# Kernel tuning notes

Measured on AMD Instinct MI355X. Metric: run time of the kernel, lower is better.

Reference implementation:

```python
import jax, jax.numpy as jnp
import numpy as np

T, H, F, E, K = 2048, 1024, 1024, 8, 2  # tokens, hidden, ffn, experts, top_k


def setup_inputs() -> dict:
    key = jax.random.key(0)
    k1, k2, k3, k4, k5 = jax.random.split(key, 5)
    hidden_states = jax.random.normal(k1, (T, H), dtype=jnp.float32)
    # router outputs: positive weights (renormalize=False in module, used as-is)
    topk_weights = jax.random.uniform(k2, (T, K), dtype=jnp.float32)
    topk_ids = jax.random.randint(k3, (T, K), 0, E, dtype=jnp.int32)
    # gate_up: (E, 2F, H) with first F rows = gate, last F rows = up
    gate_up_weight = jax.random.normal(k4, (E, 2 * F, H), dtype=jnp.float32) * 0.02
    # down: (E, H, F)
    down_weight = jax.random.normal(k5, (E, H, F), dtype=jnp.float32) * 0.02
    return {
        'hidden_states': hidden_states,
        'topk_weights': topk_weights,
        'topk_ids': topk_ids,
        'gate_up_weight': gate_up_weight,
        'down_weight': down_weight,
    }


def reference(hidden_states, topk_weights, topk_ids, gate_up_weight, down_weight):
    # Fused MoE: per selected expert, y = (silu(x@Wg^T) * (x@Wu^T)) @ Wd^T,
    # combined with router weights (renormalize=False).
    f = down_weight.shape[-1]
    # [T, E, 2F]: gate_up projection for every expert (dense ref for grouped GEMM)
    gu = jnp.einsum('th,eoh->teo', hidden_states, gate_up_weight)
    gate, up = gu[..., :f], gu[..., f:]
    act = jax.nn.silu(gate) * up                     # [T, E, F]
    y = jnp.einsum('tef,ehf->teh', act, down_weight)  # [T, E, H]
    # gather the top-k experts per token and combine
    y_sel = jnp.take_along_axis(y, topk_ids[:, :, None], axis=1)  # [T, K, H]
    out = jnp.sum(y_sel * topk_weights[:, :, None], axis=1)       # [T, H]
    return out.astype(hidden_states.dtype)
```

## Files before the change

### kernel.cpp

```cpp
#include <hip/hip_runtime.h>
#include <hip/hip_bf16.h>

#define T_TOK 2048
#define HID   1024
#define FF    1024
#define NEXP  8
#define NPAIR 4096

#define BM 128
#define BN 64
#define BK 32
#define MAX_MT 40
#define MAXROWS (MAX_MT*BM)
#define PPT (NPAIR/256)

using bf16x8 = __attribute__((ext_vector_type(8))) __bf16;
using f32x4  = __attribute__((ext_vector_type(4))) float;

__device__ __forceinline__ unsigned short f2bf(float f) {
    unsigned int u = __float_as_uint(f);
    return (unsigned short)((u + 0x7FFF + ((u >> 16) & 1)) >> 16);
}
__device__ __forceinline__ float bf2f(unsigned short s) {
    return __uint_as_float(((unsigned int)s) << 16);
}
__device__ __forceinline__ void gll16(const unsigned short* g, unsigned short* l) {
    __builtin_amdgcn_global_load_lds(
        (const __attribute__((address_space(1))) void*)(const void*)g,
        (__attribute__((address_space(3))) void*)(void*)l, 16, 0, 0);
}

__global__ void prep_kernel(const float* __restrict__ wgu,
                            const float* __restrict__ wdn,
                            const float* __restrict__ hs,
                            const int* __restrict__ ids,
                            int* __restrict__ pair_pos,
                            int* __restrict__ row_tok,
                            int* __restrict__ meta,
                            unsigned short* __restrict__ wgu_b,
                            unsigned short* __restrict__ wdn_b,
                            unsigned short* __restrict__ hs_b) {
    int tid = threadIdx.x;
    if (blockIdx.x == 2048) {
        __shared__ int S[2][256][NEXP];
        __shared__ int base[NEXP];
        int myc[NEXP];
        int eloc[PPT];
#pragma unroll
        for (int e = 0; e < NEXP; e++) myc[e] = 0;
#pragma unroll
        for (int i = 0; i < PPT; i++) {
            int e = ids[tid * PPT + i];
            eloc[i] = e;
#pragma unroll
            for (int ee = 0; ee < NEXP; ee++) myc[ee] += (e == ee);
        }
#pragma unroll
        for (int e = 0; e < NEXP; e++) S[0][tid][e] = myc[e];
        __syncthreads();
        int src = 0;
        for (int d = 1; d < 256; d <<= 1) {
#pragma unroll
            for (int e = 0; e < NEXP; e++) {
                int v = S[src][tid][e];
                if (tid >= d) v += S[src][tid - d][e];
                S[src ^ 1][tid][e] = v;
            }
            __syncthreads();
            src ^= 1;
        }
        if (tid == 0) {
            int mt = 0;
            for (int e = 0; e < NEXP; e++) {
                meta[e] = mt;
                base[e] = mt * BM;
                mt += (S[src][255][e] + BM - 1) / BM;
            }
            meta[NEXP] = mt;
        }
        for (int i = tid; i < MAXROWS; i += 256) row_tok[i] = -1;
        __syncthreads();
        int off[NEXP];
#pragma unroll
        for (int e = 0; e < NEXP; e++) off[e] = base[e] + S[src][tid][e] - myc[e];
#pragma unroll
        for (int i = 0; i < PPT; i++) {
            int p = tid * PPT + i;
            int e = eloc[i];
            int pos = 0;
#pragma unroll
            for (int ee = 0; ee < NEXP; ee++) if (e == ee) pos = off[ee]++;
            pair_pos[p] = pos;
            row_tok[pos] = p >> 1;
        }
        return;
    }
    long stride = 2048L * 256;
    long t0 = (long)blockIdx.x * 256 + tid;
    const long NW1 = (long)NEXP * 2 * FF * HID / 4;
    for (long i = t0; i < NW1; i += stride) {
        float4 v = ((const float4*)wgu)[i];
        ushort4 o; o.x = f2bf(v.x); o.y = f2bf(v.y); o.z = f2bf(v.z); o.w = f2bf(v.w);
        ((ushort4*)wgu_b)[i] = o;
    }
    const long NW2 = (long)NEXP * HID * FF / 4;
    for (long i = t0; i < NW2; i += stride) {
        float4 v = ((const float4*)wdn)[i];
        ushort4 o; o.x = f2bf(v.x); o.y = f2bf(v.y); o.z = f2bf(v.z); o.w = f2bf(v.w);
        ((ushort4*)wdn_b)[i] = o;
    }
    const long NH = (long)T_TOK * HID / 4;
    for (long i = t0; i < NH; i += stride) {
        float4 v = ((const float4*)hs)[i];
        ushort4 o; o.x = f2bf(v.x); o.y = f2bf(v.y); o.z = f2bf(v.z); o.w = f2bf(v.w);
        ((ushort4*)hs_b)[i] = o;
    }
}

template<int EPI, int NBY>
__global__ __launch_bounds__(256)
void gemm_moe(const unsigned short* __restrict__ A,
              const unsigned short* __restrict__ B,
              unsigned short* __restrict__ Cbf,
              const int* __restrict__ meta,
              const int* __restrict__ row_tok,
              int K, long Bexp) {
    __shared__ unsigned short As[2][BM * BK];
    __shared__ unsigned short Bs[2][BN * BK];

    int L = blockIdx.x;
    int xcd = L & 7;
    int slot = L >> 3;
    constexpr int PER = NBY / 8;
    int by = xcd * PER + (slot % PER);
    int bx = slot / PER;
    if (bx >= meta[NEXP]) return;
    int e = 0;
#pragma unroll
    for (int i = 1; i < NEXP; i++) if (bx >= meta[i]) e = i;

    long m0 = (long)bx * BM;
    int n0 = by * BN;
    const unsigned short* Bb = B + (long)e * Bexp;

    int tid = threadIdx.x, lane = tid & 63, wv = tid >> 6;
    const int r = lane & 15;
    const int q = lane >> 4;
    const int mw = (wv >> 1) * 64, nw = (wv & 1) * 32;
    const int sw = (q ^ ((r >> 1) & 3)) * 8;

    const unsigned short* ap[2];
#pragma unroll
    for (int h = 0; h < 2; h++) {
        int c = h * 256 + tid;
        int row = c >> 2, cp = c & 3;
        int cc = cp ^ ((row >> 1) & 3);
        long grow;
        if (EPI == 1) {
            int tk = row_tok[m0 + row];
            if (tk < 0) tk = 0;
            grow = tk;
        } else {
            grow = m0 + row;
        }
        ap[h] = A + grow * (long)K + cc * 8;
    }
    const unsigned short* bp;
    {
        int c = tid;
        int row = c >> 2, cp = c & 3;
        int cc = cp ^ ((row >> 1) & 3);
        long grow;
        if (EPI == 1) grow = ((row & 1) ? FF : 0) + ((n0 + row) >> 1);
        else          grow = n0 + row;
        bp = Bb + grow * (long)K + cc * 8;
    }

    auto stage = [&](int s, int k0) {
#pragma unroll
        for (int h = 0; h < 2; h++)
            gll16(ap[h] + k0, &As[s][(h * 256 + tid) * 8]);
        gll16(bp + k0, &Bs[s][tid * 8]);
    };

    f32x4 acc[4][2] = {};
    const int NKI = K / BK;
    stage(0, 0);
    for (int ki = 0; ki < NKI; ki++) {
        __syncthreads();
        if (ki + 1 < NKI) stage((ki + 1) & 1, (ki + 1) * BK);
        int s = ki & 1;
        bf16x8 a[4], b[2];
#pragma unroll
        for (int i = 0; i < 4; i++)
            a[i] = *(const bf16x8*)&As[s][(mw + i * 16 + r) * BK + sw];
#pragma unroll
        for (int j = 0; j < 2; j++)
            b[j] = *(const bf16x8*)&Bs[s][(nw + j * 16 + r) * BK + sw];
#pragma unroll
        for (int i = 0; i < 4; i++)
#pragma unroll
            for (int j = 0; j < 2; j++)
                acc[i][j] = __builtin_amdgcn_mfma_f32_16x16x32_bf16(a[i], b[j], acc[i][j], 0, 0, 0);
        __syncthreads();
    }

    if (EPI == 1) {
#pragma unroll
        for (int i = 0; i < 4; i++) {
            long rowb = m0 + mw + i * 16 + q * 4;
#pragma unroll
            for (int j = 0; j < 2; j++) {
                int n = n0 + nw + j * 16 + r;
#pragma unroll
                for (int reg = 0; reg < 4; reg++) {
                    float v = acc[i][j][reg];
                    float o = __shfl_xor(v, 1);
                    if (!(r & 1)) {
                        float g = v, u = o;
                        float s2 = g / (1.f + __expf(-g)) * u;
                        Cbf[(rowb + reg) * (long)FF + (n >> 1)] = f2bf(s2);
                    }
                }
            }
        }
    } else {
#pragma unroll
        for (int i = 0; i < 4; i++) {
            long rowb = m0 + mw + i * 16 + q * 4;
#pragma unroll
            for (int j = 0; j < 2; j++) {
                int n = n0 + nw + j * 16 + r;
#pragma unroll
                for (int reg = 0; reg < 4; reg++)
                    Cbf[(rowb + reg) * (long)HID + n] = f2bf(acc[i][j][reg]);
            }
        }
    }
}

__global__ void combine_kernel(const unsigned short* __restrict__ y,
                               const float* __restrict__ tw,
                               const int* __restrict__ pair_pos,
                               float* __restrict__ out) {
    int t = blockIdx.x;
    int c = threadIdx.x * 4;
    int p0 = pair_pos[t * 2], p1 = pair_pos[t * 2 + 1];
    float w0 = tw[t * 2], w1 = tw[t * 2 + 1];
    ushort4 a = *(const ushort4*)(y + (long)p0 * HID + c);
    ushort4 b = *(const ushort4*)(y + (long)p1 * HID + c);
    float4 o;
    o.x = w0 * bf2f(a.x) + w1 * bf2f(b.x);
    o.y = w0 * bf2f(a.y) + w1 * bf2f(b.y);
    o.z = w0 * bf2f(a.z) + w1 * bf2f(b.z);
    o.w = w0 * bf2f(a.w) + w1 * bf2f(b.w);
    *(float4*)(out + (long)t * HID + c) = o;
}

extern "C" void kernel_launch(void* const* d_in, const int* in_sizes, int n_in,
                              void* d_out, int out_size, void* d_ws, size_t ws_size,
                              hipStream_t stream) {
    const float* hs  = (const float*)d_in[0];
    const float* tw  = (const float*)d_in[1];
    const int*   ids = (const int*)d_in[2];
    const float* wgu = (const float*)d_in[3];
    const float* wdn = (const float*)d_in[4];
    float* out = (float*)d_out;

    char* ws = (char*)d_ws;
    size_t off = 0;
    auto alloc = [&](size_t bytes) -> void* {
        void* p = ws + off;
        off += (bytes + 255) & ~(size_t)255;
        return p;
    };
    unsigned short* wgu_b = (unsigned short*)alloc((size_t)NEXP * 2 * FF * HID * 2);
    unsigned short* wdn_b = (unsigned short*)alloc((size_t)NEXP * HID * FF * 2);
    unsigned short* hs_b  = (unsigned short*)alloc((size_t)T_TOK * HID * 2);
    unsigned short* act   = (unsigned short*)alloc((size_t)MAXROWS * FF * 2);
    unsigned short* ybuf  = (unsigned short*)alloc((size_t)MAXROWS * HID * 2);
    int* pair_pos = (int*)alloc(NPAIR * 4);
    int* row_tok  = (int*)alloc(MAXROWS * 4);
    int* meta     = (int*)alloc(64);

    prep_kernel<<<2049, 256, 0, stream>>>(wgu, wdn, hs, ids,
                                          pair_pos, row_tok, meta,
                                          wgu_b, wdn_b, hs_b);

    gemm_moe<1, 32><<<32 * MAX_MT, 256, 0, stream>>>(
        hs_b, wgu_b, act, meta, row_tok, HID, (long)(2 * FF) * HID);

    gemm_moe<2, 16><<<16 * MAX_MT, 256, 0, stream>>>(
        act, wdn_b, ybuf, meta, row_tok, FF, (long)HID * FF);

    combine_kernel<<<T_TOK, 256, 0, stream>>>(ybuf, tw, pair_pos, out);
}
```

Baseline: 205.6 us.

## Fuse fp32 weight-to-bf16 conversion into GEMM loads and widen N tile

```diff
diff --git a/kernel.cpp b/kernel.cpp
--- a/kernel.cpp
+++ b/kernel.cpp
@@ -8,13 +8,15 @@
 #define NPAIR 4096
 
 #define BM 128
-#define BN 64
+#define BN 128
 #define BK 32
 #define MAX_MT 40
 #define MAXROWS (MAX_MT*BM)
 #define PPT (NPAIR/256)
+#define NPREP 512
 
 using bf16x8 = __attribute__((ext_vector_type(8))) __bf16;
+using us8    = __attribute__((ext_vector_type(8))) unsigned short;
 using f32x4  = __attribute__((ext_vector_type(4))) float;
 
 __device__ __forceinline__ unsigned short f2bf(float f) {
@@ -24,24 +26,15 @@
 __device__ __forceinline__ float bf2f(unsigned short s) {
     return __uint_as_float(((unsigned int)s) << 16);
 }
-__device__ __forceinline__ void gll16(const unsigned short* g, unsigned short* l) {
-    __builtin_amdgcn_global_load_lds(
-        (const __attribute__((address_space(1))) void*)(const void*)g,
-        (__attribute__((address_space(3))) void*)(void*)l, 16, 0, 0);
-}
-
-__global__ void prep_kernel(const float* __restrict__ wgu,
-                            const float* __restrict__ wdn,
-                            const float* __restrict__ hs,
+
+__global__ void prep_kernel(const float* __restrict__ hs,
                             const int* __restrict__ ids,
                             int* __restrict__ pair_pos,
                             int* __restrict__ row_tok,
                             int* __restrict__ meta,
-                            unsigned short* __restrict__ wgu_b,
-                            unsigned short* __restrict__ wdn_b,
                             unsigned short* __restrict__ hs_b) {
     int tid = threadIdx.x;
-    if (blockIdx.x == 2048) {
+    if (blockIdx.x == NPREP) {
         __shared__ int S[2][256][NEXP];
         __shared__ int base[NEXP];
         int myc[NEXP];
@@ -95,22 +88,9 @@
         }
         return;
     }
-    long stride = 2048L * 256;
-    long t0 = (long)blockIdx.x * 256 + tid;
-    const long NW1 = (long)NEXP * 2 * FF * HID / 4;
-    for (long i = t0; i < NW1; i += stride) {
-        float4 v = ((const float4*)wgu)[i];
-        ushort4 o; o.x = f2bf(v.x); o.y = f2bf(v.y); o.z = f2bf(v.z); o.w = f2bf(v.w);
-        ((ushort4*)wgu_b)[i] = o;
-    }
-    const long NW2 = (long)NEXP * HID * FF / 4;
-    for (long i = t0; i < NW2; i += stride) {
-        float4 v = ((const float4*)wdn)[i];
-        ushort4 o; o.x = f2bf(v.x); o.y = f2bf(v.y); o.z = f2bf(v.z); o.w = f2bf(v.w);
-        ((ushort4*)wdn_b)[i] = o;
-    }
+    long stride = (long)NPREP * 256;
     const long NH = (long)T_TOK * HID / 4;
-    for (long i = t0; i < NH; i += stride) {
+    for (long i = (long)blockIdx.x * 256 + tid; i < NH; i += stride) {
         float4 v = ((const float4*)hs)[i];
         ushort4 o; o.x = f2bf(v.x); o.y = f2bf(v.y); o.z = f2bf(v.z); o.w = f2bf(v.w);
         ((ushort4*)hs_b)[i] = o;
@@ -120,7 +100,7 @@
 template<int EPI, int NBY>
 __global__ __launch_bounds__(256)
 void gemm_moe(const unsigned short* __restrict__ A,
-              const unsigned short* __restrict__ B,
+              const float* __restrict__ Bf,
               unsigned short* __restrict__ Cbf,
               const int* __restrict__ meta,
               const int* __restrict__ row_tok,
@@ -141,68 +121,79 @@
 
     long m0 = (long)bx * BM;
     int n0 = by * BN;
-    const unsigned short* Bb = B + (long)e * Bexp;
 
     int tid = threadIdx.x, lane = tid & 63, wv = tid >> 6;
     const int r = lane & 15;
     const int q = lane >> 4;
-    const int mw = (wv >> 1) * 64, nw = (wv & 1) * 32;
+    const int mw = (wv >> 1) * 64, nw = (wv & 1) * 64;
     const int sw = (q ^ ((r >> 1) & 3)) * 8;
 
-    const unsigned short* ap[2];
+    const unsigned short* apb[2];
+    const float* bpb[2];
 #pragma unroll
     for (int h = 0; h < 2; h++) {
         int c = h * 256 + tid;
         int row = c >> 2, cp = c & 3;
         int cc = cp ^ ((row >> 1) & 3);
-        long grow;
+        long ga, gb;
         if (EPI == 1) {
             int tk = row_tok[m0 + row];
             if (tk < 0) tk = 0;
-            grow = tk;
+            ga = tk;
+            gb = ((row & 1) ? FF : 0) + ((n0 + row) >> 1);
         } else {
-            grow = m0 + row;
-        }
-        ap[h] = A + grow * (long)K + cc * 8;
-    }
-    const unsigned short* bp;
-    {
-        int c = tid;
-        int row = c >> 2, cp = c & 3;
-        int cc = cp ^ ((row >> 1) & 3);
-        long grow;
-        if (EPI == 1) grow = ((row & 1) ? FF : 0) + ((n0 + row) >> 1);
-        else          grow = n0 + row;
-        bp = Bb + grow * (long)K + cc * 8;
-    }
-
-    auto stage = [&](int s, int k0) {
-#pragma unroll
-        for (int h = 0; h < 2; h++)
-            gll16(ap[h] + k0, &As[s][(h * 256 + tid) * 8]);
-        gll16(bp + k0, &Bs[s][tid * 8]);
+            ga = m0 + row;
+            gb = n0 + row;
+        }
+        apb[h] = A + ga * (long)K + cc * 8;
+        bpb[h] = Bf + (long)e * Bexp + gb * (long)K + cc * 8;
+    }
+
+    us8   Ar[2];
+    float4 Br[2][2];
+    auto ldregs = [&](int k0) {
+#pragma unroll
+        for (int h = 0; h < 2; h++) {
+            Ar[h]    = *(const us8*)(apb[h] + k0);
+            Br[h][0] = *(const float4*)(bpb[h] + k0);
+            Br[h][1] = *(const float4*)(bpb[h] + k0 + 4);
+        }
     };
-
-    f32x4 acc[4][2] = {};
+    auto dswrite = [&](int s) {
+#pragma unroll
+        for (int h = 0; h < 2; h++) {
+            int c = h * 256 + tid;
+            *(us8*)&As[s][c * 8] = Ar[h];
+            us8 bo;
+            float4 x = Br[h][0], y = Br[h][1];
+            bo[0] = f2bf(x.x); bo[1] = f2bf(x.y); bo[2] = f2bf(x.z); bo[3] = f2bf(x.w);
+            bo[4] = f2bf(y.x); bo[5] = f2bf(y.y); bo[6] = f2bf(y.z); bo[7] = f2bf(y.w);
+            *(us8*)&Bs[s][c * 8] = bo;
+        }
+    };
+
+    f32x4 acc[4][4] = {};
     const int NKI = K / BK;
-    stage(0, 0);
+    ldregs(0);
+    dswrite(0);
+    ldregs(BK);
     for (int ki = 0; ki < NKI; ki++) {
         __syncthreads();
-        if (ki + 1 < NKI) stage((ki + 1) & 1, (ki + 1) * BK);
         int s = ki & 1;
-        bf16x8 a[4], b[2];
+        bf16x8 a[4], b[4];
 #pragma unroll
         for (int i = 0; i < 4; i++)
             a[i] = *(const bf16x8*)&As[s][(mw + i * 16 + r) * BK + sw];
 #pragma unroll
-        for (int j = 0; j < 2; j++)
+        for (int j = 0; j < 4; j++)
             b[j] = *(const bf16x8*)&Bs[s][(nw + j * 16 + r) * BK + sw];
+        if (ki + 1 < NKI) dswrite(s ^ 1);
+        if (ki + 2 < NKI) ldregs((ki + 2) * BK);
 #pragma unroll
         for (int i = 0; i < 4; i++)
 #pragma unroll
-            for (int j = 0; j < 2; j++)
+            for (int j = 0; j < 4; j++)
                 acc[i][j] = __builtin_amdgcn_mfma_f32_16x16x32_bf16(a[i], b[j], acc[i][j], 0, 0, 0);
-        __syncthreads();
     }
 
     if (EPI == 1) {
@@ -210,7 +201,7 @@
         for (int i = 0; i < 4; i++) {
             long rowb = m0 + mw + i * 16 + q * 4;
 #pragma unroll
-            for (int j = 0; j < 2; j++) {
+            for (int j = 0; j < 4; j++) {
                 int n = n0 + nw + j * 16 + r;
 #pragma unroll
                 for (int reg = 0; reg < 4; reg++) {
@@ -229,7 +220,7 @@
         for (int i = 0; i < 4; i++) {
             long rowb = m0 + mw + i * 16 + q * 4;
 #pragma unroll
-            for (int j = 0; j < 2; j++) {
+            for (int j = 0; j < 4; j++) {
                 int n = n0 + nw + j * 16 + r;
 #pragma unroll
                 for (int reg = 0; reg < 4; reg++)
@@ -274,24 +265,20 @@
         off += (bytes + 255) & ~(size_t)255;
         return p;
     };
-    unsigned short* wgu_b = (unsigned short*)alloc((size_t)NEXP * 2 * FF * HID * 2);
-    unsigned short* wdn_b = (unsigned short*)alloc((size_t)NEXP * HID * FF * 2);
-    unsigned short* hs_b  = (unsigned short*)alloc((size_t)T_TOK * HID * 2);
-    unsigned short* act   = (unsigned short*)alloc((size_t)MAXROWS * FF * 2);
-    unsigned short* ybuf  = (unsigned short*)alloc((size_t)MAXROWS * HID * 2);
+    unsigned short* hs_b = (unsigned short*)alloc((size_t)T_TOK * HID * 2);
+    unsigned short* act  = (unsigned short*)alloc((size_t)MAXROWS * FF * 2);
+    unsigned short* ybuf = (unsigned short*)alloc((size_t)MAXROWS * HID * 2);
     int* pair_pos = (int*)alloc(NPAIR * 4);
     int* row_tok  = (int*)alloc(MAXROWS * 4);
     int* meta     = (int*)alloc(64);
 
-    prep_kernel<<<2049, 256, 0, stream>>>(wgu, wdn, hs, ids,
-                                          pair_pos, row_tok, meta,
-                                          wgu_b, wdn_b, hs_b);
-
-    gemm_moe<1, 32><<<32 * MAX_MT, 256, 0, stream>>>(
-        hs_b, wgu_b, act, meta, row_tok, HID, (long)(2 * FF) * HID);
-
-    gemm_moe<2, 16><<<16 * MAX_MT, 256, 0, stream>>>(
-        act, wdn_b, ybuf, meta, row_tok, FF, (long)HID * FF);
+    prep_kernel<<<NPREP + 1, 256, 0, stream>>>(hs, ids, pair_pos, row_tok, meta, hs_b);
+
+    gemm_moe<1, 16><<<16 * MAX_MT, 256, 0, stream>>>(
+        hs_b, wgu, act, meta, row_tok, HID, (long)(2 * FF) * HID);
+
+    gemm_moe<2, 8><<<8 * MAX_MT, 256, 0, stream>>>(
+        act, wdn, ybuf, meta, row_tok, FF, (long)HID * FF);
 
     combine_kernel<<<T_TOK, 256, 0, stream>>>(ybuf, tw, pair_pos, out);
 }
```

Result: no change. 205.7 us (+0.1%).
